# Optimization experiments

Hardware: AMD Instinct MI355X
Metric: run time of the kernel (lower is better)

The kernel has to match this reference:

```python
import jax, jax.numpy as jnp
import numpy as np

N = 100000
E = 3200000
F_IN = 512
NUM_CLASSES = 8
H1, C1 = 4, 8   # conv1: 4 heads, 8 channels each (concat -> 32)
H2, C2 = 1, NUM_CLASSES  # conv2: 1 head, mean (concat=False)
NEG_SLOPE = 0.2


def gat_conv(x, W, att_src, att_dst, bias, src, dst, num_nodes, concat):
    """PyG-style GATConv (eval mode, self-loops already in src/dst)."""
    H, C = att_src.shape
    xp = (x @ W).reshape(-1, H, C)              # [N, H, C]
    a_s = (xp * att_src[None]).sum(-1)           # [N, H]
    a_d = (xp * att_dst[None]).sum(-1)           # [N, H]
    e = jax.nn.leaky_relu(a_s[src] + a_d[dst], NEG_SLOPE)  # [E, H]
    # segment softmax over destination nodes (stable)
    e_max = jax.ops.segment_max(e, dst, num_segments=num_nodes)
    e = jnp.exp(e - e_max[dst])
    denom = jax.ops.segment_sum(e, dst, num_segments=num_nodes)
    alpha = e / denom[dst]                        # [E, H]
    msg = xp[src] * alpha[..., None]              # [E, H, C]
    out = jax.ops.segment_sum(msg, dst, num_segments=num_nodes)  # [N, H, C]
    if concat:
        out = out.reshape(num_nodes, H * C)
    else:
        out = out.mean(axis=1)
    return out + bias


def setup_inputs() -> dict:
    key = jax.random.key(0)
    ks = jax.random.split(key, 9)
    s = 0.1
    return {
        "x": jax.random.normal(ks[0], (N, F_IN), dtype=jnp.float32),
        "edge_index": jax.random.randint(ks[1], (2, E), 0, N, dtype=jnp.int32),
        "W1": jax.random.normal(ks[2], (F_IN, H1 * C1), dtype=jnp.float32) * s,
        "att_src1": jax.random.normal(ks[3], (H1, C1), dtype=jnp.float32) * s,
        "att_dst1": jax.random.normal(ks[4], (H1, C1), dtype=jnp.float32) * s,
        "b1": jnp.zeros((H1 * C1,), dtype=jnp.float32),
        "W2": jax.random.normal(ks[5], (H1 * C1, H2 * C2), dtype=jnp.float32) * s,
        "att_src2": jax.random.normal(ks[6], (H2, C2), dtype=jnp.float32) * s,
        "att_dst2": jax.random.normal(ks[7], (H2, C2), dtype=jnp.float32) * s,
        "b2": jnp.zeros((C2,), dtype=jnp.float32),
    }


def reference(x, edge_index, W1, att_src1, att_dst1, b1, W2, att_src2, att_dst2, b2):
    # PyG GATConv default add_self_loops=True
    loop = jnp.arange(N, dtype=edge_index.dtype)
    src = jnp.concatenate([edge_index[0], loop])
    dst = jnp.concatenate([edge_index[1], loop])
    # dropout is identity in eval mode
    h = jax.nn.elu(gat_conv(x, W1, att_src1, att_dst1, b1, src, dst, N, True))
    out = gat_conv(h, W2, att_src2, att_dst2, b2, src, dst, N, False)
    return out
```

## Files before the change

### kernel.cpp

```cpp
#include <hip/hip_runtime.h>

typedef unsigned short u16;
typedef unsigned int   u32;

#define NN  100000
#define EE  3200000
#define ETOT 3300000
#define FIN 512
#define NBUK 512
#define NPB  196
#define CAP  8192
#define TILE_A 8192
#define NBLK_A ((ETOT + TILE_A - 1) / TILE_A)
#define NBLK_G ((NN + 63) / 64)

typedef __attribute__((ext_vector_type(8))) short bfx8;
typedef __attribute__((ext_vector_type(4))) float f32x4;

__device__ __forceinline__ float bf2f(u16 u){ return __uint_as_float(((u32)u) << 16); }
__device__ __forceinline__ float lo16f(u32 v){ return __uint_as_float(v << 16); }
__device__ __forceinline__ float hi16f(u32 v){ return __uint_as_float(v & 0xffff0000u); }
__device__ __forceinline__ u16 f2bf(float f){
  u32 u = __float_as_uint(f);
  u += 0x7fffu + ((u >> 16) & 1u);
  return (u16)(u >> 16);
}
__device__ __forceinline__ u32 pack2(float a, float b){
  return ((u32)f2bf(b) << 16) | (u32)f2bf(a);
}

__device__ __forceinline__ void binA_body(int blk, const int* __restrict__ ei,
                                          u32* __restrict__ gcnt,
                                          u32* __restrict__ buk,
                                          u32* hcnt, u32* hbase){
  int t = threadIdx.x;
  hcnt[t] = 0; hcnt[t + 256] = 0;
  __syncthreads();
  int e0 = blk * TILE_A;
  u32 pk[32], meta[32];
  #pragma unroll
  for (int i = 0; i < 32; i++){
    int e = e0 + i*256 + t;
    if (e < ETOT){
      int s, d;
      if (e < EE){ s = ei[e]; d = ei[EE + e]; } else { s = e - EE; d = s; }
      u32 b = (u32)d / NPB;
      pk[i] = ((u32)(d - (int)b*NPB) << 17) | (u32)s;
      u32 r = atomicAdd(&hcnt[b], 1u);
      meta[i] = (b << 13) | r;
    } else meta[i] = 0xFFFFFFFFu;
  }
  __syncthreads();
  for (int q = t; q < NBUK; q += 256){
    u32 c = hcnt[q];
    if (c) hbase[q] = atomicAdd(&gcnt[q], c);
  }
  __syncthreads();
  #pragma unroll
  for (int i = 0; i < 32; i++){
    if (meta[i] != 0xFFFFFFFFu){
      u32 b = meta[i] >> 13, r = meta[i] & 8191u;
      buk[((u32)b << 13) + hbase[b] + r] = pk[i];
    }
  }
}

__device__ __forceinline__ void gemm_body(int gb,
    const float* __restrict__ x, const u16* __restrict__ WTb,
    const float* __restrict__ attS, const float* __restrict__ attD,
    u16* __restrict__ xp1, float* __restrict__ as1, float* __restrict__ ad1,
    u16* ws){
  int tid = threadIdx.x;
  int nb  = gb * 64;

  {
    int r = tid >> 3, seg = tid & 7;
    const uint4* src = (const uint4*)(WTb + r*FIN + seg*64);
    uint4* dst = (uint4*)(ws + r*520 + seg*64);
    #pragma unroll
    for (int i = 0; i < 8; i++) dst[i] = src[i];
  }
  __syncthreads();

  int lane = tid & 63, wid = tid >> 6;
  int m = lane & 15, quad = lane >> 4;
  int rowbase = wid * 16;
  int row = nb + rowbase + m; if (row >= NN) row = NN - 1;
  const float* xrow = x + (size_t)row * FIN + quad * 8;
  const u16* b0_base = ws + m * 520 + quad * 8;
  const u16* b1_base = b0_base + 16 * 520;

  f32x4 acc0 = {0.f, 0.f, 0.f, 0.f};
  f32x4 acc1 = {0.f, 0.f, 0.f, 0.f};

  union Ubf { bfx8 v; u32 u[4]; };

  #pragma unroll
  for (int kc = 0; kc < 4; kc++){
    #pragma unroll
    for (int ks = 0; ks < 4; ks++){
      const float4* g = (const float4*)(xrow + kc*128 + ks*32);
      float4 f0 = g[0], f1 = g[1];
      Ubf ua;
      ua.u[0] = pack2(f0.x, f0.y); ua.u[1] = pack2(f0.z, f0.w);
      ua.u[2] = pack2(f1.x, f1.y); ua.u[3] = pack2(f1.z, f1.w);
      bfx8 b0 = *(const bfx8*)(b0_base + kc*128 + ks*32);
      bfx8 b1 = *(const bfx8*)(b1_base + kc*128 + ks*32);
      acc0 = __builtin_amdgcn_mfma_f32_16x16x32_bf16(ua.v, b0, acc0, 0, 0, 0);
      acc1 = __builtin_amdgcn_mfma_f32_16x16x32_bf16(ua.v, b1, acc1, 0, 0, 0);
    }
  }

  #pragma unroll
  for (int t = 0; t < 2; t++){
    f32x4 acc = t ? acc1 : acc0;
    int colg = t*16 + m;
    float aS = attS[colg], aD = attD[colg];
    #pragma unroll
    for (int r = 0; r < 4; r++){
      int node = nb + rowbase + quad*4 + r;
      float v = acc[r];
      if (node < NN) xp1[(size_t)node*32 + colg] = f2bf(v);
      float ps = v * aS, pd = v * aD;
      ps += __shfl_xor(ps, 1); ps += __shfl_xor(ps, 2); ps += __shfl_xor(ps, 4);
      pd += __shfl_xor(pd, 1); pd += __shfl_xor(pd, 2); pd += __shfl_xor(pd, 4);
      if ((m & 7) == 0 && node < NN){
        as1[node*4 + (colg >> 3)] = ps;
        ad1[node*4 + (colg >> 3)] = pd;
      }
    }
  }
}


__global__ void __launch_bounds__(256) k_fat(const int* __restrict__ ei,
    u32* __restrict__ gcnt, u32* __restrict__ buk,
    const float* __restrict__ x, const u16* __restrict__ WTb,
    const float* __restrict__ attS, const float* __restrict__ attD,
    u16* __restrict__ xp1, float* __restrict__ as1, float* __restrict__ ad1){
  __shared__ __align__(16) char sm[32 * 520 * 2];
  if (blockIdx.x < NBLK_A)
    binA_body(blockIdx.x, ei, gcnt, buk, (u32*)sm, (u32*)sm + NBUK);
  else
    gemm_body(blockIdx.x - NBLK_A, x, WTb, attS, attD, xp1, as1, ad1, (u16*)sm);
}

__global__ void __launch_bounds__(256) k_binA(const int* __restrict__ ei,
                                              u32* __restrict__ gcnt,
                                              u32* __restrict__ buk){
  __shared__ u32 sm2[NBUK*2];
  binA_body(blockIdx.x, ei, gcnt, buk, sm2, sm2 + NBUK);
}

__global__ void __launch_bounds__(256) k_gemm1(
    const float* __restrict__ x, const u16* __restrict__ WTb,
    const float* __restrict__ attS, const float* __restrict__ attD,
    u16* __restrict__ xp1, float* __restrict__ as1, float* __restrict__ ad1){
  __shared__ u16 ws[32 * 520];
  gemm_body(blockIdx.x, x, WTb, attS, attD, xp1, as1, ad1, ws);
}

__global__ void __launch_bounds__(256) k_scatterB(const u32* __restrict__ gcnt,
                                                  const u32* __restrict__ buk,
                                                  int2* __restrict__ range,
                                                  int* __restrict__ srcs){
  __shared__ u32 dcnt[NPB + 1];
  __shared__ u32 cur[NPB];
  __shared__ u32 red[256];
  int b = blockIdx.x, t = threadIdx.x;
  u32 acc = 0;
  for (int i = t; i < b; i += 256) acc += gcnt[i];
  red[t] = acc;
  if (t < NPB + 1) dcnt[t] = 0;
  __syncthreads();
  for (int o = 128; o > 0; o >>= 1){
    if (t < o) red[t] += red[t + o];
    __syncthreads();
  }
  u32 gb = red[0];
  u32 lo = (u32)b << 13;
  u32 hi = lo + gcnt[b];
  for (u32 j = lo + t; j < hi; j += 256)
    atomicAdd(&dcnt[(buk[j] >> 17) + 1], 1u);
  __syncthreads();
  for (int o = 1; o < 256; o <<= 1){
    u32 x = 0;
    if (t < NPB + 1 && t >= o) x = dcnt[t - o];
    __syncthreads();
    if (t < NPB + 1 && t >= o) dcnt[t] += x;
    __syncthreads();
  }
  if (t < NPB){
    u32 beg = gb + dcnt[t];
    cur[t] = beg;
    int node = b * NPB + t;
    if (node < NN){
      range[node] = make_int2((int)beg, (int)(gb + dcnt[t + 1]));
    }
  }
  __syncthreads();
  for (u32 j = lo + t; j < hi; j += 256){
    u32 p = buk[j];
    u32 pos = atomicAdd(&cur[p >> 17], 1u);
    srcs[pos] = (int)(p & 0x1FFFFu);
  }
}

__global__ void k_prep_w(const float* __restrict__ W1, u16* __restrict__ WTb,
                         u32* __restrict__ gcnt){
  int i = blockIdx.x*blockDim.x + threadIdx.x;
  if (i < NBUK) gcnt[i] = 0;
  if (i >= FIN*32) return;
  int k = i >> 5, c = i & 31;
  WTb[c*FIN + k] = f2bf(W1[i]);
}

__global__ void __launch_bounds__(256) k_agg1(
    const int2* __restrict__ range, const int* __restrict__ srcs,
    const u32* __restrict__ xp1u, const float* __restrict__ as1,
    const float* __restrict__ ad1, const float* __restrict__ b1,
    u32* __restrict__ hfeatu){
  int wid = (blockIdx.x * 256 + threadIdx.x) >> 6;
  if (wid >= NN) return;
  int lane = threadIdx.x & 63;
  int e = lane >> 4;
  int l = lane & 15;
  int h = l >> 2;
  int2 rr = range[wid];
  int beg = rr.x, end = rr.y;
  float ad = ad1[wid*4 + h];
  float num0 = 0.f, num1 = 0.f, den = 0.f;
  int j = beg + e;
  for (; j + 4 < end; j += 8){
    int s0 = srcs[j], s1 = srcs[j + 4];
    u32 v0 = xp1u[(size_t)s0*16 + l];
    u32 v1 = xp1u[(size_t)s1*16 + l];
    float z0 = as1[s0*4 + h] + ad;
    float z1 = as1[s1*4 + h] + ad;
    z0 = (z0 >= 0.f) ? z0 : 0.2f * z0;
    z1 = (z1 >= 0.f) ? z1 : 0.2f * z1;
    float w0 = __expf(z0), w1 = __expf(z1);
    num0 = fmaf(w0, lo16f(v0), num0); num1 = fmaf(w0, hi16f(v0), num1); den += w0;
    num0 = fmaf(w1, lo16f(v1), num0); num1 = fmaf(w1, hi16f(v1), num1); den += w1;
  }
  for (; j < end; j += 4){
    int s0 = srcs[j];
    u32 v0 = xp1u[(size_t)s0*16 + l];
    float z0 = as1[s0*4 + h] + ad;
    z0 = (z0 >= 0.f) ? z0 : 0.2f * z0;
    float w0 = __expf(z0);
    num0 = fmaf(w0, lo16f(v0), num0); num1 = fmaf(w0, hi16f(v0), num1); den += w0;
  }
  num0 += __shfl_xor(num0, 16); num0 += __shfl_xor(num0, 32);
  num1 += __shfl_xor(num1, 16); num1 += __shfl_xor(num1, 32);
  den  += __shfl_xor(den, 16);  den  += __shfl_xor(den, 32);
  if (e == 0){
    float o0 = num0 / den + b1[2*l];
    float o1 = num1 / den + b1[2*l + 1];
    o0 = (o0 > 0.f) ? o0 : (__expf(o0) - 1.f);
    o1 = (o1 > 0.f) ? o1 : (__expf(o1) - 1.f);
    hfeatu[(size_t)wid*16 + l] = pack2(o0, o1);
  }
}

__global__ void k_feat2(const u16* __restrict__ hfeat, const float* __restrict__ W2,
                        const float* __restrict__ attS, const float* __restrict__ attD,
                        float* __restrict__ xp2, float* __restrict__ as2,
                        float* __restrict__ ad2){
  int n = blockIdx.x*blockDim.x + threadIdx.x;
  if (n >= NN) return;
  const u16* hr = hfeat + (size_t)n*32;
  float h[32];
  #pragma unroll
  for (int k = 0; k < 32; k++) h[k] = bf2f(hr[k]);
  float o[8];
  #pragma unroll
  for (int j = 0; j < 8; j++) o[j] = 0.f;
  #pragma unroll
  for (int k = 0; k < 32; k++){
    #pragma unroll
    for (int j = 0; j < 8; j++) o[j] = fmaf(h[k], W2[k*8 + j], o[j]);
  }
  float s = 0.f, d = 0.f;
  #pragma unroll
  for (int j = 0; j < 8; j++){
    xp2[(size_t)n*8 + j] = o[j];
    s = fmaf(o[j], attS[j], s);
    d = fmaf(o[j], attD[j], d);
  }
  as2[n] = s; ad2[n] = d;
}

__global__ void __launch_bounds__(256) k_agg2(
    const int2* __restrict__ range, const int* __restrict__ srcs,
    const float* __restrict__ xp2, const float* __restrict__ as2,
    const float* __restrict__ ad2, const float* __restrict__ b2,
    float* __restrict__ out){
  int wid = (blockIdx.x * 256 + threadIdx.x) >> 6;
  if (wid >= NN) return;
  int lane = threadIdx.x & 63;
  int p = lane >> 3, c = lane & 7;
  int2 rr = range[wid];
  int beg = rr.x, end = rr.y;
  float ad = ad2[wid];
  float num = 0.f, den = 0.f;
  int j = beg + p;
  for (; j + 8 < end; j += 16){
    int s0 = srcs[j], s1 = srcs[j + 8];
    float v0 = xp2[(size_t)s0*8 + c];
    float v1 = xp2[(size_t)s1*8 + c];
    float z0 = as2[s0] + ad;
    float z1 = as2[s1] + ad;
    z0 = (z0 >= 0.f) ? z0 : 0.2f * z0;
    z1 = (z1 >= 0.f) ? z1 : 0.2f * z1;
    float w0 = __expf(z0), w1 = __expf(z1);
    num = fmaf(w0, v0, num); den += w0;
    num = fmaf(w1, v1, num); den += w1;
  }
  for (; j < end; j += 8){
    int s0 = srcs[j];
    float v0 = xp2[(size_t)s0*8 + c];
    float z0 = as2[s0] + ad;
    z0 = (z0 >= 0.f) ? z0 : 0.2f * z0;
    float w0 = __expf(z0);
    num = fmaf(w0, v0, num); den += w0;
  }
  num += __shfl_xor(num, 8);  den += __shfl_xor(den, 8);
  num += __shfl_xor(num, 16); den += __shfl_xor(den, 16);
  num += __shfl_xor(num, 32); den += __shfl_xor(den, 32);
  if (p == 0){
    out[(size_t)wid*8 + c] = num / den + b2[c];
  }
}

extern "C" void kernel_launch(void* const* d_in, const int* in_sizes, int n_in,
                              void* d_out, int out_size, void* d_ws, size_t ws_size,
                              hipStream_t stream){
  (void)in_sizes; (void)n_in; (void)out_size;
  const float* x   = (const float*)d_in[0];
  const int*   ei  = (const int*)d_in[1];
  const float* W1  = (const float*)d_in[2];
  const float* aS1 = (const float*)d_in[3];
  const float* aD1 = (const float*)d_in[4];
  const float* b1  = (const float*)d_in[5];
  const float* W2  = (const float*)d_in[6];
  const float* aS2 = (const float*)d_in[7];
  const float* aD2 = (const float*)d_in[8];
  const float* b2  = (const float*)d_in[9];
  float* out = (float*)d_out;

  char* w = (char*)d_ws;
  auto alloc = [&](size_t bytes) -> char* {
    char* p = w; w += (bytes + 15) & ~(size_t)15; return p;
  };

  int2*  range  = (int2*)alloc((size_t)NN*8);
  int*   srcs   = (int*)alloc((size_t)ETOT*4);
  u16*   xp1    = (u16*)alloc((size_t)NN*64);
  float* as1    = (float*)alloc((size_t)NN*16);
  float* ad1    = (float*)alloc((size_t)NN*16);
  u16*   hfeat  = (u16*)alloc((size_t)NN*64);
  float* xp2    = (float*)alloc((size_t)NN*32);
  float* as2    = (float*)alloc((size_t)NN*4);
  float* ad2    = (float*)alloc((size_t)NN*4);
  u16*   WTb    = (u16*)alloc(32*512*2);
  u32*   gcnt   = (u32*)alloc(NBUK*4);
  size_t base_need = (size_t)(w - (char*)d_ws);
  size_t buk_bytes = (size_t)NBUK * CAP * 4;
  bool overlap = (ws_size >= base_need + buk_bytes);

  u32* buk;
  if (overlap){
    buk = (u32*)alloc(buk_bytes);
  } else {
    buk = (u32*)xp1;
  }

  k_prep_w  <<<64, 256, 0, stream>>>(W1, WTb, gcnt);
  if (overlap){
    k_fat   <<<NBLK_A + NBLK_G, 256, 0, stream>>>(ei, gcnt, buk, x, WTb, aS1, aD1,
                                                  xp1, as1, ad1);
    k_scatterB<<<NBUK, 256, 0, stream>>>(gcnt, buk, range, srcs);
  } else {
    k_binA  <<<NBLK_A, 256, 0, stream>>>(ei, gcnt, buk);
    k_scatterB<<<NBUK, 256, 0, stream>>>(gcnt, buk, range, srcs);
    k_gemm1 <<<NBLK_G, 256, 0, stream>>>(x, WTb, aS1, aD1, xp1, as1, ad1);
  }
  k_agg1    <<<NN/4, 256, 0, stream>>>(range, srcs, (const u32*)xp1, as1, ad1, b1, (u32*)hfeat);
  k_feat2   <<<(NN+255)/256, 256, 0, stream>>>(hfeat, W2, aS2, aD2, xp2, as2, ad2);
  k_agg2    <<<NN/4, 256, 0, stream>>>(range, srcs, xp2, as2, ad2, b2, out);
}
```

Before: 487.2 us.

## Shrink bucket size, drop LDS weight staging in GEMM, deepen aggregation unroll

Doubles the number of destination buckets (half the nodes per bucket, half the capacity) so each scatter block handles a smaller segment and needs fewer prefix-scan steps. The GEMM no longer stages the bf16 weight matrix in LDS and reads it directly from global/cache, which shrinks shared memory in the fused kernel. Launch bounds now request higher occupancy. Both aggregation kernels unroll the edge loop 4-wide to keep more gathers in flight. The risks are extra uncached weight traffic in the GEMM and bucket overflow if a bucket exceeds 4096 edges (the mean is about 3200).

```diff
diff --git a/kernel.cpp b/kernel.cpp
--- a/kernel.cpp
+++ b/kernel.cpp
@@ -7,9 +7,9 @@
 #define EE  3200000
 #define ETOT 3300000
 #define FIN 512
-#define NBUK 512
-#define NPB  196
-#define CAP  8192
+#define NBUK 1024
+#define NPB  98
+#define CAP  4096
 #define TILE_A 8192
 #define NBLK_A ((ETOT + TILE_A - 1) / TILE_A)
 #define NBLK_G ((NN + 63) / 64)
@@ -34,7 +34,7 @@
                                           u32* __restrict__ buk,
                                           u32* hcnt, u32* hbase){
   int t = threadIdx.x;
-  hcnt[t] = 0; hcnt[t + 256] = 0;
+  hcnt[t] = 0; hcnt[t + 256] = 0; hcnt[t + 512] = 0; hcnt[t + 768] = 0;
   __syncthreads();
   int e0 = blk * TILE_A;
   u32 pk[32], meta[32];
@@ -47,7 +47,7 @@
       u32 b = (u32)d / NPB;
       pk[i] = ((u32)(d - (int)b*NPB) << 17) | (u32)s;
       u32 r = atomicAdd(&hcnt[b], 1u);
-      meta[i] = (b << 13) | r;
+      meta[i] = (b << 12) | r;
     } else meta[i] = 0xFFFFFFFFu;
   }
   __syncthreads();
@@ -59,8 +59,8 @@
   #pragma unroll
   for (int i = 0; i < 32; i++){
     if (meta[i] != 0xFFFFFFFFu){
-      u32 b = meta[i] >> 13, r = meta[i] & 8191u;
-      buk[((u32)b << 13) + hbase[b] + r] = pk[i];
+      u32 b = meta[i] >> 12, r = meta[i] & 4095u;
+      buk[((u32)b << 12) + hbase[b] + r] = pk[i];
     }
   }
 }
@@ -68,27 +68,17 @@
 __device__ __forceinline__ void gemm_body(int gb,
     const float* __restrict__ x, const u16* __restrict__ WTb,
     const float* __restrict__ attS, const float* __restrict__ attD,
-    u16* __restrict__ xp1, float* __restrict__ as1, float* __restrict__ ad1,
-    u16* ws){
+    u16* __restrict__ xp1, float* __restrict__ as1, float* __restrict__ ad1){
   int tid = threadIdx.x;
   int nb  = gb * 64;
-
-  {
-    int r = tid >> 3, seg = tid & 7;
-    const uint4* src = (const uint4*)(WTb + r*FIN + seg*64);
-    uint4* dst = (uint4*)(ws + r*520 + seg*64);
-    #pragma unroll
-    for (int i = 0; i < 8; i++) dst[i] = src[i];
-  }
-  __syncthreads();
 
   int lane = tid & 63, wid = tid >> 6;
   int m = lane & 15, quad = lane >> 4;
   int rowbase = wid * 16;
   int row = nb + rowbase + m; if (row >= NN) row = NN - 1;
   const float* xrow = x + (size_t)row * FIN + quad * 8;
-  const u16* b0_base = ws + m * 520 + quad * 8;
-  const u16* b1_base = b0_base + 16 * 520;
+  const u16* b0g = WTb + m * FIN + quad * 8;
+  const u16* b1g = b0g + 16 * FIN;
 
   f32x4 acc0 = {0.f, 0.f, 0.f, 0.f};
   f32x4 acc1 = {0.f, 0.f, 0.f, 0.f};
@@ -104,8 +94,8 @@
       Ubf ua;
       ua.u[0] = pack2(f0.x, f0.y); ua.u[1] = pack2(f0.z, f0.w);
       ua.u[2] = pack2(f1.x, f1.y); ua.u[3] = pack2(f1.z, f1.w);
-      bfx8 b0 = *(const bfx8*)(b0_base + kc*128 + ks*32);
-      bfx8 b1 = *(const bfx8*)(b1_base + kc*128 + ks*32);
+      bfx8 b0 = *(const bfx8*)(b0g + kc*128 + ks*32);
+      bfx8 b1 = *(const bfx8*)(b1g + kc*128 + ks*32);
       acc0 = __builtin_amdgcn_mfma_f32_16x16x32_bf16(ua.v, b0, acc0, 0, 0, 0);
       acc1 = __builtin_amdgcn_mfma_f32_16x16x32_bf16(ua.v, b1, acc1, 0, 0, 0);
     }
@@ -133,16 +123,16 @@
 }
 
 
-__global__ void __launch_bounds__(256) k_fat(const int* __restrict__ ei,
+__global__ void __launch_bounds__(256, 8) k_fat(const int* __restrict__ ei,
     u32* __restrict__ gcnt, u32* __restrict__ buk,
     const float* __restrict__ x, const u16* __restrict__ WTb,
     const float* __restrict__ attS, const float* __restrict__ attD,
     u16* __restrict__ xp1, float* __restrict__ as1, float* __restrict__ ad1){
-  __shared__ __align__(16) char sm[32 * 520 * 2];
+  __shared__ u32 sm[NBUK*2];
   if (blockIdx.x < NBLK_A)
-    binA_body(blockIdx.x, ei, gcnt, buk, (u32*)sm, (u32*)sm + NBUK);
+    binA_body(blockIdx.x, ei, gcnt, buk, sm, sm + NBUK);
   else
-    gemm_body(blockIdx.x - NBLK_A, x, WTb, attS, attD, xp1, as1, ad1, (u16*)sm);
+    gemm_body(blockIdx.x - NBLK_A, x, WTb, attS, attD, xp1, as1, ad1);
 }
 
 __global__ void __launch_bounds__(256) k_binA(const int* __restrict__ ei,
@@ -152,12 +142,11 @@
   binA_body(blockIdx.x, ei, gcnt, buk, sm2, sm2 + NBUK);
 }
 
-__global__ void __launch_bounds__(256) k_gemm1(
+__global__ void __launch_bounds__(256, 8) k_gemm1(
     const float* __restrict__ x, const u16* __restrict__ WTb,
     const float* __restrict__ attS, const float* __restrict__ attD,
     u16* __restrict__ xp1, float* __restrict__ as1, float* __restrict__ ad1){
-  __shared__ u16 ws[32 * 520];
-  gemm_body(blockIdx.x, x, WTb, attS, attD, xp1, as1, ad1, ws);
+  gemm_body(blockIdx.x, x, WTb, attS, attD, xp1, as1, ad1);
 }
 
 __global__ void __launch_bounds__(256) k_scatterB(const u32* __restrict__ gcnt,
@@ -178,12 +167,12 @@
     __syncthreads();
   }
   u32 gb = red[0];
-  u32 lo = (u32)b << 13;
+  u32 lo = (u32)b << 12;
   u32 hi = lo + gcnt[b];
   for (u32 j = lo + t; j < hi; j += 256)
     atomicAdd(&dcnt[(buk[j] >> 17) + 1], 1u);
   __syncthreads();
-  for (int o = 1; o < 256; o <<= 1){
+  for (int o = 1; o < 128; o <<= 1){
     u32 x = 0;
     if (t < NPB + 1 && t >= o) x = dcnt[t - o];
     __syncthreads();
@@ -231,7 +220,27 @@
   float ad = ad1[wid*4 + h];
   float num0 = 0.f, num1 = 0.f, den = 0.f;
   int j = beg + e;
-  for (; j + 4 < end; j += 8){
+  for (; j + 12 < end; j += 16){
+    int s0 = srcs[j], s1 = srcs[j + 4], s2 = srcs[j + 8], s3 = srcs[j + 12];
+    u32 v0 = xp1u[(size_t)s0*16 + l];
+    u32 v1 = xp1u[(size_t)s1*16 + l];
+    u32 v2 = xp1u[(size_t)s2*16 + l];
+    u32 v3 = xp1u[(size_t)s3*16 + l];
+    float z0 = as1[s0*4 + h] + ad;
+    float z1 = as1[s1*4 + h] + ad;
+    float z2 = as1[s2*4 + h] + ad;
+    float z3 = as1[s3*4 + h] + ad;
+    z0 = (z0 >= 0.f) ? z0 : 0.2f * z0;
+    z1 = (z1 >= 0.f) ? z1 : 0.2f * z1;
+    z2 = (z2 >= 0.f) ? z2 : 0.2f * z2;
+    z3 = (z3 >= 0.f) ? z3 : 0.2f * z3;
+    float w0 = __expf(z0), w1 = __expf(z1), w2 = __expf(z2), w3 = __expf(z3);
+    num0 = fmaf(w0, lo16f(v0), num0); num1 = fmaf(w0, hi16f(v0), num1); den += w0;
+    num0 = fmaf(w1, lo16f(v1), num0); num1 = fmaf(w1, hi16f(v1), num1); den += w1;
+    num0 = fmaf(w2, lo16f(v2), num0); num1 = fmaf(w2, hi16f(v2), num1); den += w2;
+    num0 = fmaf(w3, lo16f(v3), num0); num1 = fmaf(w3, hi16f(v3), num1); den += w3;
+  }
+  if (j + 4 < end){
     int s0 = srcs[j], s1 = srcs[j + 4];
     u32 v0 = xp1u[(size_t)s0*16 + l];
     u32 v1 = xp1u[(size_t)s1*16 + l];
@@ -242,6 +251,7 @@
     float w0 = __expf(z0), w1 = __expf(z1);
     num0 = fmaf(w0, lo16f(v0), num0); num1 = fmaf(w0, hi16f(v0), num1); den += w0;
     num0 = fmaf(w1, lo16f(v1), num0); num1 = fmaf(w1, hi16f(v1), num1); den += w1;
+    j += 8;
   }
   for (; j < end; j += 4){
     int s0 = srcs[j];
@@ -305,7 +315,27 @@
   float ad = ad2[wid];
   float num = 0.f, den = 0.f;
   int j = beg + p;
-  for (; j + 8 < end; j += 16){
+  for (; j + 24 < end; j += 32){
+    int s0 = srcs[j], s1 = srcs[j + 8], s2 = srcs[j + 16], s3 = srcs[j + 24];
+    float v0 = xp2[(size_t)s0*8 + c];
+    float v1 = xp2[(size_t)s1*8 + c];
+    float v2 = xp2[(size_t)s2*8 + c];
+    float v3 = xp2[(size_t)s3*8 + c];
+    float z0 = as2[s0] + ad;
+    float z1 = as2[s1] + ad;
+    float z2 = as2[s2] + ad;
+    float z3 = as2[s3] + ad;
+    z0 = (z0 >= 0.f) ? z0 : 0.2f * z0;
+    z1 = (z1 >= 0.f) ? z1 : 0.2f * z1;
+    z2 = (z2 >= 0.f) ? z2 : 0.2f * z2;
+    z3 = (z3 >= 0.f) ? z3 : 0.2f * z3;
+    float w0 = __expf(z0), w1 = __expf(z1), w2 = __expf(z2), w3 = __expf(z3);
+    num = fmaf(w0, v0, num); den += w0;
+    num = fmaf(w1, v1, num); den += w1;
+    num = fmaf(w2, v2, num); den += w2;
+    num = fmaf(w3, v3, num); den += w3;
+  }
+  if (j + 8 < end){
     int s0 = srcs[j], s1 = srcs[j + 8];
     float v0 = xp2[(size_t)s0*8 + c];
     float v1 = xp2[(size_t)s1*8 + c];
@@ -316,6 +346,7 @@
     float w0 = __expf(z0), w1 = __expf(z1);
     num = fmaf(w0, v0, num); den += w0;
     num = fmaf(w1, v1, num); den += w1;
+    j += 16;
   }
   for (; j < end; j += 8){
     int s0 = srcs[j];
```

Result: slower. 499.2 us (+2.5%).
